# Kernel tuning notes

Hardware: AMD Instinct MI355X
Metric: run time of the kernel (lower is better)

Reference implementation:

```python
import math
import jax, jax.numpy as jnp
import numpy as np

E = 1024
H = 16
HD = E // H
MLP = 4 * E
EPS = 1e-6


def setup_inputs() -> dict:
    key = jax.random.key(0)
    ks = jax.random.split(key, 12)
    s = lambda fan_in: 1.0 / math.sqrt(fan_in)
    return {
        "x": jax.random.normal(ks[0], (8, 1024, E), dtype=jnp.float32),
        "ln1_g": jnp.ones((E,), jnp.float32),
        "ln1_b": jnp.zeros((E,), jnp.float32),
        "w_qkv": jax.random.normal(ks[1], (E, 3 * E), jnp.float32) * s(E),
        "b_qkv": jnp.zeros((3 * E,), jnp.float32),
        "w_o": jax.random.normal(ks[2], (E, E), jnp.float32) * s(E),
        "b_o": jnp.zeros((E,), jnp.float32),
        "ln2_g": jnp.ones((E,), jnp.float32),
        "ln2_b": jnp.zeros((E,), jnp.float32),
        "w_fc1": jax.random.normal(ks[3], (E, MLP), jnp.float32) * s(E),
        "b_fc1": jnp.zeros((MLP,), jnp.float32),
        "w_fc2": jax.random.normal(ks[4], (MLP, E), jnp.float32) * s(MLP),
        "b_fc2": jnp.zeros((E,), jnp.float32),
    }


def _layernorm(x, g, b):
    mu = jnp.mean(x, axis=-1, keepdims=True)
    var = jnp.mean(jnp.square(x - mu), axis=-1, keepdims=True)
    return (x - mu) * jax.lax.rsqrt(var + EPS) * g + b


def _attn(x, w_qkv, b_qkv, w_o, b_o):
    B, N, _ = x.shape
    qkv = (x @ w_qkv + b_qkv).reshape(B, N, 3, H, HD)
    q, k, v = qkv[:, :, 0], qkv[:, :, 1], qkv[:, :, 2]  # [B,N,H,HD]
    scores = jnp.einsum("bnhd,bmhd->bhnm", q, k) / math.sqrt(HD)
    probs = jax.nn.softmax(scores, axis=-1)
    out = jnp.einsum("bhnm,bmhd->bnhd", probs, v).reshape(B, N, H * HD)
    return out @ w_o + b_o


def reference(x, ln1_g, ln1_b, w_qkv, b_qkv, w_o, b_o, ln2_g, ln2_b,
              w_fc1, b_fc1, w_fc2, b_fc2):
    # pre-LN attention block with residual
    x = x + _attn(_layernorm(x, ln1_g, ln1_b), w_qkv, b_qkv, w_o, b_o)
    # pre-LN MLP block with residual (exact GELU, matching torch nn.GELU)
    h = _layernorm(x, ln2_g, ln2_b) @ w_fc1 + b_fc1
    h = jax.nn.gelu(h, approximate=False)
    x = x + (h @ w_fc2 + b_fc2)
    return x
```

## Files before the change

### kernel.cpp

```cpp
#include <hip/hip_runtime.h>
#include <stdint.h>

typedef unsigned short u16;
typedef __bf16 bf16x8 __attribute__((ext_vector_type(8)));
typedef float f32x4 __attribute__((ext_vector_type(4)));

#define GLD16(gp, lp) __builtin_amdgcn_global_load_lds( \
    (__attribute__((address_space(1))) void*)(uintptr_t)(gp), \
    (__attribute__((address_space(3))) void*)(uintptr_t)(lp), 16, 0, 0)

#define MM(a, b, c) __builtin_amdgcn_mfma_f32_16x16x32_bf16(a, b, c, 0, 0, 0)

__device__ __forceinline__ u16 f2bf(float f) {
  uint32_t u = __builtin_bit_cast(uint32_t, f);
  u += 0x7FFFu + ((u >> 16) & 1u);
  return (u16)(u >> 16);
}

__global__ __launch_bounds__(256) void wtrans(const float* __restrict__ w,
                                              u16* __restrict__ wt, int K, int Nn) {
  __shared__ float tile[64][68];
  const int c0 = blockIdx.x << 6, r0 = blockIdx.y << 6;
  const int t = threadIdx.x, tr = t >> 2, tc = t & 3;
#pragma unroll
  for (int p = 0; p < 4; ++p) {
    float4 v = *(const float4*)&w[(size_t)(r0 + tr) * Nn + c0 + tc * 4 + p * 16];
    tile[tr][tc * 4 + p * 16 + 0] = v.x;
    tile[tr][tc * 4 + p * 16 + 1] = v.y;
    tile[tr][tc * 4 + p * 16 + 2] = v.z;
    tile[tr][tc * 4 + p * 16 + 3] = v.w;
  }
  __syncthreads();
#pragma unroll
  for (int p = 0; p < 4; ++p) {
    u16 e0 = f2bf(tile[tc * 4 + p * 16 + 0][tr]);
    u16 e1 = f2bf(tile[tc * 4 + p * 16 + 1][tr]);
    u16 e2 = f2bf(tile[tc * 4 + p * 16 + 2][tr]);
    u16 e3 = f2bf(tile[tc * 4 + p * 16 + 3][tr]);
    uint2 o;
    o.x = (uint32_t)e0 | ((uint32_t)e1 << 16);
    o.y = (uint32_t)e2 | ((uint32_t)e3 << 16);
    *(uint2*)&wt[(size_t)(c0 + tr) * K + r0 + tc * 4 + p * 16] = o;
  }
}

__global__ __launch_bounds__(256) void lnorm(const float* x, const float* __restrict__ g,
                                             const float* __restrict__ bta,
                                             u16* __restrict__ out) {
  const int lane = threadIdx.x & 63, wid = threadIdx.x >> 6;
  const size_t token = (size_t)blockIdx.x * 4 + wid;
  const float* row = x + token * 1024;
  float v[16];
#pragma unroll
  for (int i = 0; i < 4; ++i) {
    float4 f = *(const float4*)&row[(lane + i * 64) * 4];
    v[i * 4 + 0] = f.x; v[i * 4 + 1] = f.y; v[i * 4 + 2] = f.z; v[i * 4 + 3] = f.w;
  }
  float s = 0.f, s2 = 0.f;
#pragma unroll
  for (int i = 0; i < 16; ++i) { s += v[i]; s2 += v[i] * v[i]; }
  for (int off = 1; off < 64; off <<= 1) {
    s += __shfl_xor(s, off);
    s2 += __shfl_xor(s2, off);
  }
  const float mu = s * (1.0f / 1024.0f);
  const float var = s2 * (1.0f / 1024.0f) - mu * mu;
  const float rstd = rsqrtf(var + 1e-6f);
  u16* orow = out + token * 1024;
#pragma unroll
  for (int i = 0; i < 4; ++i) {
    const int c = (lane + i * 64) * 4;
    float4 gv = *(const float4*)&g[c];
    float4 bv = *(const float4*)&bta[c];
    u16 e0 = f2bf((v[i * 4 + 0] - mu) * rstd * gv.x + bv.x);
    u16 e1 = f2bf((v[i * 4 + 1] - mu) * rstd * gv.y + bv.y);
    u16 e2 = f2bf((v[i * 4 + 2] - mu) * rstd * gv.z + bv.z);
    u16 e3 = f2bf((v[i * 4 + 3] - mu) * rstd * gv.w + bv.w);
    uint2 o;
    o.x = (uint32_t)e0 | ((uint32_t)e1 << 16);
    o.y = (uint32_t)e2 | ((uint32_t)e3 << 16);
    *(uint2*)&orow[c] = o;
  }
}

template <int EPI>
__global__ __launch_bounds__(256, 4) void g97(const u16* __restrict__ A,
                                              const u16* __restrict__ Bt,
                                              const float* __restrict__ bias,
                                              const float* res, void* Cout,
                                              int Ndim, int K, float qscale,
                                              int qlimit, int gn) {
  __shared__ __align__(16) u16 lds[2][8192];
  const int tid = threadIdx.x, lane = tid & 63, wid = tid >> 6;
  const int wm = wid & 1, wn = wid >> 1;

  const int wg = blockIdx.x;
  const int swz = (wg & 7) * ((int)gridDim.x >> 3) + (wg >> 3);
  const int mblk = swz / gn, nb = swz - mblk * gn;
  const int m0 = mblk << 7, n0 = nb << 7;

  const int srow = tid >> 2;
  const int gsub = (tid & 3) ^ ((tid >> 3) & 3);
  const u16* Ag = A + (size_t)(m0 + srow) * K + gsub * 8;
  const u16* Bg = Bt + (size_t)(n0 + srow) * K + gsub * 8;
  const size_t rstep = (size_t)64 * K;
  char* lb = (char*)&lds[0][0];

  const int rrow = lane & 15, g = lane >> 4;
  const int xg = g ^ ((rrow >> 1) & 3);
  const int aoff = (wm * 64 + rrow) * 64 + xg * 16;
  const int boff = 8192 + (wn * 64 + rrow) * 64 + xg * 16;

  const f32x4 fzero = {0.f, 0.f, 0.f, 0.f};
  f32x4 acc[4][4];
#pragma unroll
  for (int i = 0; i < 4; ++i)
#pragma unroll
    for (int j = 0; j < 4; ++j) acc[i][j] = fzero;

#define STG(kt, s) do { \
    char* d_ = lb + (s) * 16384; \
    GLD16(Ag + (size_t)(kt) * 32, d_ + tid * 16); \
    GLD16(Ag + rstep + (size_t)(kt) * 32, d_ + 4096 + tid * 16); \
    GLD16(Bg + (size_t)(kt) * 32, d_ + 8192 + tid * 16); \
    GLD16(Bg + rstep + (size_t)(kt) * 32, d_ + 12288 + tid * 16); \
  } while (0)

  const int nk = K >> 5;
  STG(0, 0);
  __syncthreads();
  for (int kt = 0; kt < nk; ++kt) {
    if (kt + 1 < nk) STG(kt + 1, (kt + 1) & 1);
    const char* sb = lb + (kt & 1) * 16384;
    bf16x8 af[4], bfr[4];
#pragma unroll
    for (int mf = 0; mf < 4; ++mf)
      af[mf] = *(const bf16x8*)(sb + aoff + mf * 1024);
#pragma unroll
    for (int nf = 0; nf < 4; ++nf)
      bfr[nf] = *(const bf16x8*)(sb + boff + nf * 1024);
#pragma unroll
    for (int mf = 0; mf < 4; ++mf)
#pragma unroll
      for (int nf = 0; nf < 4; ++nf)
        acc[mf][nf] = MM(af[mf], bfr[nf], acc[mf][nf]);
    __syncthreads();
  }
#undef STG

  const int g4 = (lane >> 4) << 2;
#pragma unroll
  for (int nf = 0; nf < 4; ++nf) {
    const int col = n0 + wn * 64 + nf * 16 + rrow;
    const float bvb = bias[col];
    const float csf = (EPI == 0 && col < qlimit) ? qscale : 1.0f;
#pragma unroll
    for (int mf = 0; mf < 4; ++mf) {
#pragma unroll
      for (int r = 0; r < 4; ++r) {
        const int row = m0 + wm * 64 + mf * 16 + g4 + r;
        float v = acc[mf][nf][r] + bvb;
        if (EPI == 0) v *= csf;
        if (EPI == 1) v = 0.5f * v * (1.0f + erff(v * 0.70710678118654752f));
        if (EPI == 2) {
          v += res[(size_t)row * Ndim + col];
          ((float*)Cout)[(size_t)row * Ndim + col] = v;
        } else {
          ((u16*)Cout)[(size_t)row * Ndim + col] = f2bf(v);
        }
      }
    }
  }
}

__global__ __launch_bounds__(256) void vtrans(const u16* __restrict__ qkv,
                                              u16* __restrict__ vt) {
  const int bh = blockIdx.y, b = bh >> 4, h = bh & 15;
  const int n0 = blockIdx.x << 6;
  __shared__ __align__(16) u16 tile[64][72];
  const int t = threadIdx.x, r = t >> 2, c = t & 3;
  const u16* src = qkv + (size_t)((b << 10) + n0 + r) * 3072 + 2048 + (h << 6);
#pragma unroll
  for (int p = 0; p < 2; ++p)
    *(uint4*)&tile[r][(c * 2 + p) * 8] = *(const uint4*)(src + (c * 2 + p) * 8);
  __syncthreads();
  u16* dst = vt + (size_t)((bh << 6) + r) * 1024 + n0;
#pragma unroll
  for (int p = 0; p < 2; ++p) {
    u16 o[8];
#pragma unroll
    for (int j = 0; j < 8; ++j) o[j] = tile[(c * 2 + p) * 8 + j][r];
    uint4 w;
    w.x = (uint32_t)o[0] | ((uint32_t)o[1] << 16);
    w.y = (uint32_t)o[2] | ((uint32_t)o[3] << 16);
    w.z = (uint32_t)o[4] | ((uint32_t)o[5] << 16);
    w.w = (uint32_t)o[6] | ((uint32_t)o[7] << 16);
    *(uint4*)&dst[(c * 2 + p) * 8] = w;
  }
}

__global__ __launch_bounds__(256) void attn64(const u16* __restrict__ qkv,
                                              const u16* __restrict__ vt,
                                              u16* __restrict__ aout) {
  const int bh = blockIdx.y, b = bh >> 4, h = bh & 15;
  const int q0 = blockIdx.x << 6;
  const int tid = threadIdx.x, lane = tid & 63, wid = tid >> 6;
  __shared__ __align__(16) u16 kl[4096];
  __shared__ __align__(16) u16 vl[4096];
  __shared__ __align__(16) u16 pl[4][1152];

  const int rrow = lane & 15;
  const int g = lane >> 4;
  const u16* qrow = qkv + (size_t)((b << 10) + q0 + (wid << 4) + rrow) * 3072 + (h << 6);
  bf16x8 qf0 = *(const bf16x8*)(qrow + (g << 3));
  bf16x8 qf1 = *(const bf16x8*)(qrow + 32 + (g << 3));

  const int sr = lane >> 3;
  const int lc = (lane & 7) ^ sr;
  const u16* kbase = qkv + (size_t)(b << 10) * 3072 + 1024 + (h << 6) +
                     (size_t)(16 * wid + sr) * 3072 + lc * 8;
  const u16* vbase = vt + (size_t)(bh << 6) * 1024 + (size_t)(16 * wid + sr) * 1024 + lc * 8;

  const f32x4 fzero = {0.f, 0.f, 0.f, 0.f};
  f32x4 oacc[4];
#pragma unroll
  for (int i = 0; i < 4; ++i) oacc[i] = fzero;
  f32x4 lacc = fzero;
  const int rcb = lane & 7;
  u16* plw = &pl[wid][0];

  for (int t = 0; t < 16; ++t) {
    const int kt0 = t << 6;
    GLD16(kbase + (size_t)kt0 * 3072, &kl[(2 * wid + 0) * 512]);
    GLD16(kbase + (size_t)kt0 * 3072 + 8 * 3072, &kl[(2 * wid + 1) * 512]);
    GLD16(vbase + kt0, &vl[(2 * wid + 0) * 512]);
    GLD16(vbase + kt0 + 8 * 1024, &vl[(2 * wid + 1) * 512]);
    __syncthreads();

    f32x4 s4[4];
#pragma unroll
    for (int i = 0; i < 4; ++i) s4[i] = fzero;
#pragma unroll
    for (int nf = 0; nf < 4; ++nf) {
      bf16x8 k0 = *(const bf16x8*)((const char*)kl + (nf * 16 + rrow) * 128 +
                                   ((g + 0) ^ rcb) * 16);
      bf16x8 k1 = *(const bf16x8*)((const char*)kl + (nf * 16 + rrow) * 128 +
                                   ((g + 4) ^ rcb) * 16);
      s4[nf] = __builtin_amdgcn_mfma_f32_16x16x32_bf16(k0, qf0, s4[nf], 0, 0, 0);
      s4[nf] = __builtin_amdgcn_mfma_f32_16x16x32_bf16(k1, qf1, s4[nf], 0, 0, 0);
    }

#pragma unroll
    for (int nf = 0; nf < 4; ++nf) {
      float p0 = exp2f(s4[nf][0]);
      float p1 = exp2f(s4[nf][1]);
      float p2 = exp2f(s4[nf][2]);
      float p3 = exp2f(s4[nf][3]);
      f32x4 pv = {p0, p1, p2, p3};
      lacc += pv;
      uint32_t a0 = __builtin_bit_cast(uint32_t, p0) + 0x8000u;
      uint32_t a1 = __builtin_bit_cast(uint32_t, p1) + 0x8000u;
      uint32_t a2 = __builtin_bit_cast(uint32_t, p2) + 0x8000u;
      uint32_t a3 = __builtin_bit_cast(uint32_t, p3) + 0x8000u;
      uint2 w;
      w.x = __builtin_amdgcn_perm(a1, a0, 0x07060302);
      w.y = __builtin_amdgcn_perm(a3, a2, 0x07060302);
      *(uint2*)(plw + rrow * 72 + nf * 16 + (g << 2)) = w;
    }

    bf16x8 pf0 = *(const bf16x8*)((const char*)plw + rrow * 144 + (g << 4));
    bf16x8 pf1 = *(const bf16x8*)((const char*)plw + rrow * 144 + (g << 4) + 64);
#pragma unroll
    for (int nf = 0; nf < 4; ++nf) {
      bf16x8 v0 = *(const bf16x8*)((const char*)vl + (nf * 16 + rrow) * 128 +
                                   ((g + 0) ^ rcb) * 16);
      bf16x8 v1 = *(const bf16x8*)((const char*)vl + (nf * 16 + rrow) * 128 +
                                   ((g + 4) ^ rcb) * 16);
      oacc[nf] = __builtin_amdgcn_mfma_f32_16x16x32_bf16(pf0, v0, oacc[nf], 0, 0, 0);
      oacc[nf] = __builtin_amdgcn_mfma_f32_16x16x32_bf16(pf1, v1, oacc[nf], 0, 0, 0);
    }
    __syncthreads();
  }

  float lsum = lacc[0] + lacc[1] + lacc[2] + lacc[3];
  lsum += __shfl_xor(lsum, 16);
  lsum += __shfl_xor(lsum, 32);
  const float inv = 1.0f / lsum;
  float invq[4];
#pragma unroll
  for (int r = 0; r < 4; ++r) {
    int bi = __builtin_amdgcn_ds_bpermute(((g << 2) + r) << 2,
                                          __builtin_bit_cast(int, inv));
    invq[r] = __builtin_bit_cast(float, bi);
  }
  u16* ob = aout + (size_t)((b << 10) + q0 + (wid << 4)) * 1024 + (h << 6);
#pragma unroll
  for (int nf = 0; nf < 4; ++nf)
#pragma unroll
    for (int r = 0; r < 4; ++r)
      ob[(size_t)(g * 4 + r) * 1024 + nf * 16 + rrow] = f2bf(oacc[nf][r] * invq[r]);
}

extern "C" void kernel_launch(void* const* d_in, const int* in_sizes, int n_in,
                              void* d_out, int out_size, void* d_ws, size_t ws_size,
                              hipStream_t stream) {
  const float* x = (const float*)d_in[0];
  const float* ln1_g = (const float*)d_in[1];
  const float* ln1_b = (const float*)d_in[2];
  const float* w_qkv = (const float*)d_in[3];
  const float* b_qkv = (const float*)d_in[4];
  const float* w_o = (const float*)d_in[5];
  const float* b_o = (const float*)d_in[6];
  const float* ln2_g = (const float*)d_in[7];
  const float* ln2_b = (const float*)d_in[8];
  const float* w_fc1 = (const float*)d_in[9];
  const float* b_fc1 = (const float*)d_in[10];
  const float* w_fc2 = (const float*)d_in[11];
  const float* b_fc2 = (const float*)d_in[12];
  float* out = (float*)d_out;

  char* w = (char*)d_ws;
  u16* wqkvT = (u16*)w; w += (size_t)3072 * 1024 * 2;
  u16* woT   = (u16*)w; w += (size_t)1024 * 1024 * 2;
  u16* wfc1T = (u16*)w; w += (size_t)4096 * 1024 * 2;
  u16* wfc2T = (u16*)w; w += (size_t)1024 * 4096 * 2;
  u16* xn    = (u16*)w; w += (size_t)8192 * 1024 * 2;
  u16* qkvb  = (u16*)w; w += (size_t)8192 * 3072 * 2;
  u16* vtb   = (u16*)w; w += (size_t)128 * 64 * 1024 * 2;
  u16* attnb = (u16*)w; w += (size_t)8192 * 1024 * 2;
  u16* hbuf  = qkvb;

  const float QS = 0.18033688011112042f;

  wtrans<<<dim3(48, 16), 256, 0, stream>>>(w_qkv, wqkvT, 1024, 3072);
  wtrans<<<dim3(16, 16), 256, 0, stream>>>(w_o, woT, 1024, 1024);
  wtrans<<<dim3(64, 16), 256, 0, stream>>>(w_fc1, wfc1T, 1024, 4096);
  wtrans<<<dim3(16, 64), 256, 0, stream>>>(w_fc2, wfc2T, 4096, 1024);

  lnorm<<<2048, 256, 0, stream>>>(x, ln1_g, ln1_b, xn);
  g97<0><<<1536, 256, 0, stream>>>(xn, wqkvT, b_qkv, nullptr, qkvb, 3072, 1024, QS, 1024, 24);
  vtrans<<<dim3(16, 128), 256, 0, stream>>>(qkvb, vtb);
  attn64<<<dim3(16, 128), 256, 0, stream>>>(qkvb, vtb, attnb);
  g97<2><<<512, 256, 0, stream>>>(attnb, woT, b_o, x, out, 1024, 1024, 1.f, 0, 8);
  lnorm<<<2048, 256, 0, stream>>>(out, ln2_g, ln2_b, xn);
  g97<1><<<2048, 256, 0, stream>>>(xn, wfc1T, b_fc1, nullptr, hbuf, 4096, 1024, 1.f, 0, 32);
  g97<2><<<512, 256, 0, stream>>>(hbuf, wfc2T, b_fc2, out, out, 1024, 4096, 1.f, 0, 8);
}
```

Measured before the change: 414.1 us.

## Double GEMM K-tile depth to 64 with wider swizzled LDS layout

The bf16 GEMM kernel now stages a K-slice of 64 per iteration instead of 32. Each iteration's tile doubles to 32 KB of LDS per buffer, with a new 8-chunk XOR swizzle and two MFMA sub-steps. This halves the number of loop iterations and __syncthreads barriers per output tile, amortizing sync and issue overhead. In exchange, LDS use grows to 64 KB per block and the launch-bounds occupancy hint drops from 4 to 2 blocks per CU, which reduces latency hiding.

```diff
diff --git a/kernel.cpp b/kernel.cpp
--- a/kernel.cpp
+++ b/kernel.cpp
@@ -84,13 +84,13 @@
 }
 
 template <int EPI>
-__global__ __launch_bounds__(256, 4) void g97(const u16* __restrict__ A,
+__global__ __launch_bounds__(256, 2) void g97(const u16* __restrict__ A,
                                               const u16* __restrict__ Bt,
                                               const float* __restrict__ bias,
                                               const float* res, void* Cout,
                                               int Ndim, int K, float qscale,
                                               int qlimit, int gn) {
-  __shared__ __align__(16) u16 lds[2][8192];
+  __shared__ __align__(16) u16 lds[2][16384];
   const int tid = threadIdx.x, lane = tid & 63, wid = tid >> 6;
   const int wm = wid & 1, wn = wid >> 1;
 
@@ -99,17 +99,19 @@
   const int mblk = swz / gn, nb = swz - mblk * gn;
   const int m0 = mblk << 7, n0 = nb << 7;
 
-  const int srow = tid >> 2;
-  const int gsub = (tid & 3) ^ ((tid >> 3) & 3);
-  const u16* Ag = A + (size_t)(m0 + srow) * K + gsub * 8;
-  const u16* Bg = Bt + (size_t)(n0 + srow) * K + gsub * 8;
-  const size_t rstep = (size_t)64 * K;
+  const int srow = tid >> 3;
+  const int schunk = (tid & 7) ^ (srow & 7);
+  const u16* Ag = A + (size_t)(m0 + srow) * K + schunk * 8;
+  const u16* Bg = Bt + (size_t)(n0 + srow) * K + schunk * 8;
+  const size_t rstep = (size_t)32 * K;
   char* lb = (char*)&lds[0][0];
 
   const int rrow = lane & 15, g = lane >> 4;
-  const int xg = g ^ ((rrow >> 1) & 3);
-  const int aoff = (wm * 64 + rrow) * 64 + xg * 16;
-  const int boff = 8192 + (wn * 64 + rrow) * 64 + xg * 16;
+  const int ph0 = (g ^ (rrow & 7)) * 16;
+  const int aoff0 = (wm * 64 + rrow) * 128 + ph0;
+  const int aoff1 = (wm * 64 + rrow) * 128 + (ph0 ^ 64);
+  const int boff0 = 16384 + (wn * 64 + rrow) * 128 + ph0;
+  const int boff1 = 16384 + (wn * 64 + rrow) * 128 + (ph0 ^ 64);
 
   const f32x4 fzero = {0.f, 0.f, 0.f, 0.f};
   f32x4 acc[4][4];
@@ -119,26 +121,43 @@
     for (int j = 0; j < 4; ++j) acc[i][j] = fzero;
 
 #define STG(kt, s) do { \
-    char* d_ = lb + (s) * 16384; \
-    GLD16(Ag + (size_t)(kt) * 32, d_ + tid * 16); \
-    GLD16(Ag + rstep + (size_t)(kt) * 32, d_ + 4096 + tid * 16); \
-    GLD16(Bg + (size_t)(kt) * 32, d_ + 8192 + tid * 16); \
-    GLD16(Bg + rstep + (size_t)(kt) * 32, d_ + 12288 + tid * 16); \
+    char* d_ = lb + (s) * 32768; \
+    const u16* a_ = Ag + (size_t)(kt) * 64; \
+    const u16* b_ = Bg + (size_t)(kt) * 64; \
+    GLD16(a_,             d_ + tid * 16); \
+    GLD16(a_ + rstep,     d_ + 4096 + tid * 16); \
+    GLD16(a_ + 2 * rstep, d_ + 8192 + tid * 16); \
+    GLD16(a_ + 3 * rstep, d_ + 12288 + tid * 16); \
+    GLD16(b_,             d_ + 16384 + tid * 16); \
+    GLD16(b_ + rstep,     d_ + 20480 + tid * 16); \
+    GLD16(b_ + 2 * rstep, d_ + 24576 + tid * 16); \
+    GLD16(b_ + 3 * rstep, d_ + 28672 + tid * 16); \
   } while (0)
 
-  const int nk = K >> 5;
+  const int nk = K >> 6;
   STG(0, 0);
   __syncthreads();
   for (int kt = 0; kt < nk; ++kt) {
     if (kt + 1 < nk) STG(kt + 1, (kt + 1) & 1);
-    const char* sb = lb + (kt & 1) * 16384;
+    const char* sb = lb + (kt & 1) * 32768;
     bf16x8 af[4], bfr[4];
 #pragma unroll
     for (int mf = 0; mf < 4; ++mf)
-      af[mf] = *(const bf16x8*)(sb + aoff + mf * 1024);
+      af[mf] = *(const bf16x8*)(sb + aoff0 + mf * 2048);
 #pragma unroll
     for (int nf = 0; nf < 4; ++nf)
-      bfr[nf] = *(const bf16x8*)(sb + boff + nf * 1024);
+      bfr[nf] = *(const bf16x8*)(sb + boff0 + nf * 2048);
+#pragma unroll
+    for (int mf = 0; mf < 4; ++mf)
+#pragma unroll
+      for (int nf = 0; nf < 4; ++nf)
+        acc[mf][nf] = MM(af[mf], bfr[nf], acc[mf][nf]);
+#pragma unroll
+    for (int mf = 0; mf < 4; ++mf)
+      af[mf] = *(const bf16x8*)(sb + aoff1 + mf * 2048);
+#pragma unroll
+    for (int nf = 0; nf < 4; ++nf)
+      bfr[nf] = *(const bf16x8*)(sb + boff1 + nf * 2048);
 #pragma unroll
     for (int mf = 0; mf < 4; ++mf)
 #pragma unroll
```

New measurement: 408.6 us. About the same (-1.3%).

## Restructure GEMM to 2-wave blocks with A fragments from global and double-buffer attention K/V

Applied to the files above, without the earlier changes.

The GEMM kernel now uses 128 threads (2 waves). Each wave computes a 128x64 tile, loading A fragments straight from global memory into registers and staging only B in LDS, with a 64-wide K step and register double-buffering of A. The attention kernel double-buffers its K/V LDS tiles so the next tile's loads overlap compute, removing one barrier per iteration. The intent is to cut LDS traffic and barrier stalls. The cost is doubled accumulator registers, uncoalesced per-lane global A reads, and fewer waves per block, which may hurt latency hiding.

```diff
diff --git a/kernel.cpp b/kernel.cpp
--- a/kernel.cpp
+++ b/kernel.cpp
@@ -84,81 +84,100 @@
 }
 
 template <int EPI>
-__global__ __launch_bounds__(256, 4) void g97(const u16* __restrict__ A,
-                                              const u16* __restrict__ Bt,
-                                              const float* __restrict__ bias,
-                                              const float* res, void* Cout,
-                                              int Ndim, int K, float qscale,
-                                              int qlimit, int gn) {
-  __shared__ __align__(16) u16 lds[2][8192];
-  const int tid = threadIdx.x, lane = tid & 63, wid = tid >> 6;
-  const int wm = wid & 1, wn = wid >> 1;
+__global__ __launch_bounds__(128, 2) void gflat(const u16* __restrict__ A,
+                                                const u16* __restrict__ Bt,
+                                                const float* __restrict__ bias,
+                                                const float* res, void* Cout,
+                                                int Ndim, int K, float qscale,
+                                                int qlimit, int gn) {
+  __shared__ __align__(16) u16 ldsB[2][8192];
+  const int tid = threadIdx.x, lane = tid & 63, wn = tid >> 6;
 
   const int wg = blockIdx.x;
   const int swz = (wg & 7) * ((int)gridDim.x >> 3) + (wg >> 3);
   const int mblk = swz / gn, nb = swz - mblk * gn;
   const int m0 = mblk << 7, n0 = nb << 7;
 
-  const int srow = tid >> 2;
-  const int gsub = (tid & 3) ^ ((tid >> 3) & 3);
-  const u16* Ag = A + (size_t)(m0 + srow) * K + gsub * 8;
-  const u16* Bg = Bt + (size_t)(n0 + srow) * K + gsub * 8;
-  const size_t rstep = (size_t)64 * K;
-  char* lb = (char*)&lds[0][0];
+  const int srow = tid >> 3;
+  const int schunk = (tid & 7) ^ ((tid >> 3) & 7);
+  const u16* Bg = Bt + (size_t)(n0 + srow) * K + schunk * 8;
+  const size_t brstep = (size_t)16 * K;
 
   const int rrow = lane & 15, g = lane >> 4;
-  const int xg = g ^ ((rrow >> 1) & 3);
-  const int aoff = (wm * 64 + rrow) * 64 + xg * 16;
-  const int boff = 8192 + (wn * 64 + rrow) * 64 + xg * 16;
+  const int boff0 = (wn * 64 + rrow) * 128 + ((g ^ (rrow & 7)) * 16);
+  const int boff1 = boff0 ^ 64;
+  const u16* Ab = A + (size_t)(m0 + rrow) * K + g * 8;
+  const size_t afstep = (size_t)16 * K;
 
   const f32x4 fzero = {0.f, 0.f, 0.f, 0.f};
-  f32x4 acc[4][4];
-#pragma unroll
-  for (int i = 0; i < 4; ++i)
+  f32x4 acc[8][4];
+#pragma unroll
+  for (int i = 0; i < 8; ++i)
 #pragma unroll
     for (int j = 0; j < 4; ++j) acc[i][j] = fzero;
 
-#define STG(kt, s) do { \
-    char* d_ = lb + (s) * 16384; \
-    GLD16(Ag + (size_t)(kt) * 32, d_ + tid * 16); \
-    GLD16(Ag + rstep + (size_t)(kt) * 32, d_ + 4096 + tid * 16); \
-    GLD16(Bg + (size_t)(kt) * 32, d_ + 8192 + tid * 16); \
-    GLD16(Bg + rstep + (size_t)(kt) * 32, d_ + 12288 + tid * 16); \
+#define STGB(kt, s) do { \
+    char* d_ = (char*)&ldsB[s][0]; \
+    const u16* b_ = Bg + (size_t)(kt) * 64; \
+    GLD16(b_ + 0 * brstep, d_ + 0 * 2048 + tid * 16); \
+    GLD16(b_ + 1 * brstep, d_ + 1 * 2048 + tid * 16); \
+    GLD16(b_ + 2 * brstep, d_ + 2 * 2048 + tid * 16); \
+    GLD16(b_ + 3 * brstep, d_ + 3 * 2048 + tid * 16); \
+    GLD16(b_ + 4 * brstep, d_ + 4 * 2048 + tid * 16); \
+    GLD16(b_ + 5 * brstep, d_ + 5 * 2048 + tid * 16); \
+    GLD16(b_ + 6 * brstep, d_ + 6 * 2048 + tid * 16); \
+    GLD16(b_ + 7 * brstep, d_ + 7 * 2048 + tid * 16); \
   } while (0)
 
-  const int nk = K >> 5;
-  STG(0, 0);
+#define LDA(arr, kc) do { \
+    const u16* ap_ = Ab + (size_t)(kc) * 32; \
+    _Pragma("unroll") \
+    for (int mf_ = 0; mf_ < 8; ++mf_) arr[mf_] = *(const uint4*)(ap_ + mf_ * afstep); \
+  } while (0)
+
+#define MMPH(arr, bbase) do { \
+    bf16x8 bf_[4]; \
+    _Pragma("unroll") \
+    for (int nf_ = 0; nf_ < 4; ++nf_) \
+      bf_[nf_] = *(const bf16x8*)(sb + (bbase) + nf_ * 2048); \
+    _Pragma("unroll") \
+    for (int mf_ = 0; mf_ < 8; ++mf_) { \
+      bf16x8 av_ = __builtin_bit_cast(bf16x8, arr[mf_]); \
+      _Pragma("unroll") \
+      for (int nf_ = 0; nf_ < 4; ++nf_) \
+        acc[mf_][nf_] = MM(av_, bf_[nf_], acc[mf_][nf_]); \
+    } \
+  } while (0)
+
+  uint4 a0[8], a1[8];
+  const int nk = K >> 6;
+  STGB(0, 0);
+  LDA(a0, 0);
   __syncthreads();
   for (int kt = 0; kt < nk; ++kt) {
-    if (kt + 1 < nk) STG(kt + 1, (kt + 1) & 1);
-    const char* sb = lb + (kt & 1) * 16384;
-    bf16x8 af[4], bfr[4];
-#pragma unroll
-    for (int mf = 0; mf < 4; ++mf)
-      af[mf] = *(const bf16x8*)(sb + aoff + mf * 1024);
-#pragma unroll
-    for (int nf = 0; nf < 4; ++nf)
-      bfr[nf] = *(const bf16x8*)(sb + boff + nf * 1024);
-#pragma unroll
-    for (int mf = 0; mf < 4; ++mf)
-#pragma unroll
-      for (int nf = 0; nf < 4; ++nf)
-        acc[mf][nf] = MM(af[mf], bfr[nf], acc[mf][nf]);
+    if (kt + 1 < nk) STGB(kt + 1, (kt + 1) & 1);
+    LDA(a1, 2 * kt + 1);
+    const char* sb = (const char*)&ldsB[kt & 1][0];
+    MMPH(a0, boff0);
+    if (kt + 1 < nk) LDA(a0, 2 * kt + 2);
+    MMPH(a1, boff1);
     __syncthreads();
   }
-#undef STG
-
-  const int g4 = (lane >> 4) << 2;
+#undef STGB
+#undef LDA
+#undef MMPH
+
+  const int g4 = g << 2;
 #pragma unroll
   for (int nf = 0; nf < 4; ++nf) {
     const int col = n0 + wn * 64 + nf * 16 + rrow;
     const float bvb = bias[col];
     const float csf = (EPI == 0 && col < qlimit) ? qscale : 1.0f;
 #pragma unroll
-    for (int mf = 0; mf < 4; ++mf) {
+    for (int mf = 0; mf < 8; ++mf) {
 #pragma unroll
       for (int r = 0; r < 4; ++r) {
-        const int row = m0 + wm * 64 + mf * 16 + g4 + r;
+        const int row = m0 + mf * 16 + g4 + r;
         float v = acc[mf][nf][r] + bvb;
         if (EPI == 0) v *= csf;
         if (EPI == 1) v = 0.5f * v * (1.0f + erff(v * 0.70710678118654752f));
@@ -205,8 +224,8 @@
   const int bh = blockIdx.y, b = bh >> 4, h = bh & 15;
   const int q0 = blockIdx.x << 6;
   const int tid = threadIdx.x, lane = tid & 63, wid = tid >> 6;
-  __shared__ __align__(16) u16 kl[4096];
-  __shared__ __align__(16) u16 vl[4096];
+  __shared__ __align__(16) u16 kl[2][4096];
+  __shared__ __align__(16) u16 vl[2][4096];
   __shared__ __align__(16) u16 pl[4][1152];
 
   const int rrow = lane & 15;
@@ -229,23 +248,28 @@
   const int rcb = lane & 7;
   u16* plw = &pl[wid][0];
 
+#define ASTAGE(t, s) do { \
+    const int kt0_ = (t) << 6; \
+    GLD16(kbase + (size_t)kt0_ * 3072, &kl[s][(2 * wid + 0) * 512]); \
+    GLD16(kbase + (size_t)kt0_ * 3072 + 8 * 3072, &kl[s][(2 * wid + 1) * 512]); \
+    GLD16(vbase + kt0_, &vl[s][(2 * wid + 0) * 512]); \
+    GLD16(vbase + kt0_ + 8 * 1024, &vl[s][(2 * wid + 1) * 512]); \
+  } while (0)
+
+  ASTAGE(0, 0);
+  __syncthreads();
   for (int t = 0; t < 16; ++t) {
-    const int kt0 = t << 6;
-    GLD16(kbase + (size_t)kt0 * 3072, &kl[(2 * wid + 0) * 512]);
-    GLD16(kbase + (size_t)kt0 * 3072 + 8 * 3072, &kl[(2 * wid + 1) * 512]);
-    GLD16(vbase + kt0, &vl[(2 * wid + 0) * 512]);
-    GLD16(vbase + kt0 + 8 * 1024, &vl[(2 * wid + 1) * 512]);
-    __syncthreads();
+    if (t + 1 < 16) ASTAGE(t + 1, (t + 1) & 1);
+    const char* klp = (const char*)&kl[t & 1][0];
+    const char* vlp = (const char*)&vl[t & 1][0];
 
     f32x4 s4[4];
 #pragma unroll
     for (int i = 0; i < 4; ++i) s4[i] = fzero;
 #pragma unroll
     for (int nf = 0; nf < 4; ++nf) {
-      bf16x8 k0 = *(const bf16x8*)((const char*)kl + (nf * 16 + rrow) * 128 +
-                                   ((g + 0) ^ rcb) * 16);
-      bf16x8 k1 = *(const bf16x8*)((const char*)kl + (nf * 16 + rrow) * 128 +
-                                   ((g + 4) ^ rcb) * 16);
+      bf16x8 k0 = *(const bf16x8*)(klp + (nf * 16 + rrow) * 128 + ((g + 0) ^ rcb) * 16);
+      bf16x8 k1 = *(const bf16x8*)(klp + (nf * 16 + rrow) * 128 + ((g + 4) ^ rcb) * 16);
       s4[nf] = __builtin_amdgcn_mfma_f32_16x16x32_bf16(k0, qf0, s4[nf], 0, 0, 0);
       s4[nf] = __builtin_amdgcn_mfma_f32_16x16x32_bf16(k1, qf1, s4[nf], 0, 0, 0);
     }
@@ -272,15 +296,14 @@
     bf16x8 pf1 = *(const bf16x8*)((const char*)plw + rrow * 144 + (g << 4) + 64);
 #pragma unroll
     for (int nf = 0; nf < 4; ++nf) {
-      bf16x8 v0 = *(const bf16x8*)((const char*)vl + (nf * 16 + rrow) * 128 +
-                                   ((g + 0) ^ rcb) * 16);
-      bf16x8 v1 = *(const bf16x8*)((const char*)vl + (nf * 16 + rrow) * 128 +
-                                   ((g + 4) ^ rcb) * 16);
+      bf16x8 v0 = *(const bf16x8*)(vlp + (nf * 16 + rrow) * 128 + ((g + 0) ^ rcb) * 16);
+      bf16x8 v1 = *(const bf16x8*)(vlp + (nf * 16 + rrow) * 128 + ((g + 4) ^ rcb) * 16);
       oacc[nf] = __builtin_amdgcn_mfma_f32_16x16x32_bf16(pf0, v0, oacc[nf], 0, 0, 0);
       oacc[nf] = __builtin_amdgcn_mfma_f32_16x16x32_bf16(pf1, v1, oacc[nf], 0, 0, 0);
     }
     __syncthreads();
   }
+#undef ASTAGE
 
   float lsum = lacc[0] + lacc[1] + lacc[2] + lacc[3];
   lsum += __shfl_xor(lsum, 16);
@@ -338,11 +361,11 @@
   wtrans<<<dim3(16, 64), 256, 0, stream>>>(w_fc2, wfc2T, 4096, 1024);
 
   lnorm<<<2048, 256, 0, stream>>>(x, ln1_g, ln1_b, xn);
-  g97<0><<<1536, 256, 0, stream>>>(xn, wqkvT, b_qkv, nullptr, qkvb, 3072, 1024, QS, 1024, 24);
+  gflat<0><<<1536, 128, 0, stream>>>(xn, wqkvT, b_qkv, nullptr, qkvb, 3072, 1024, QS, 1024, 24);
   vtrans<<<dim3(16, 128), 256, 0, stream>>>(qkvb, vtb);
   attn64<<<dim3(16, 128), 256, 0, stream>>>(qkvb, vtb, attnb);
-  g97<2><<<512, 256, 0, stream>>>(attnb, woT, b_o, x, out, 1024, 1024, 1.f, 0, 8);
+  gflat<2><<<512, 128, 0, stream>>>(attnb, woT, b_o, x, out, 1024, 1024, 1.f, 0, 8);
   lnorm<<<2048, 256, 0, stream>>>(out, ln2_g, ln2_b, xn);
-  g97<1><<<2048, 256, 0, stream>>>(xn, wfc1T, b_fc1, nullptr, hbuf, 4096, 1024, 1.f, 0, 32);
-  g97<2><<<512, 256, 0, stream>>>(hbuf, wfc2T, b_fc2, out, out, 1024, 4096, 1.f, 0, 8);
-}
+  gflat<1><<<2048, 128, 0, stream>>>(xn, wfc1T, b_fc1, nullptr, hbuf, 4096, 1024, 1.f, 0, 32);
+  gflat<2><<<512, 128, 0, stream>>>(hbuf, wfc2T, b_fc2, out, out, 1024, 4096, 1.f, 0, 8);
+}
```

Result: slower. 684.3 us (+65.2%).

## Enlarge GEMM tile to 256x128 and double-buffer attention K/V loads

Applied to the files above, without the earlier changes.

The GEMM kernel now computes a 256x128 output tile per block, with each wave covering 128x64 (8x4 MFMA fragments). This raises arithmetic intensity per LDS load and halves the grid sizes, at the cost of more accumulator registers and lower occupancy (launch bounds drop to 2 blocks per CU). Separately, the attention kernel double-buffers its K/V LDS tiles so the next tile's global-to-LDS loads overlap the current tile's compute. With only 256 blocks, the Wo and fc2 GEMMs may leave some of the 256 CUs underfilled.

```diff
diff --git a/kernel.cpp b/kernel.cpp
--- a/kernel.cpp
+++ b/kernel.cpp
@@ -84,20 +84,20 @@
 }
 
 template <int EPI>
-__global__ __launch_bounds__(256, 4) void g97(const u16* __restrict__ A,
+__global__ __launch_bounds__(256, 2) void gwt(const u16* __restrict__ A,
                                               const u16* __restrict__ Bt,
                                               const float* __restrict__ bias,
                                               const float* res, void* Cout,
                                               int Ndim, int K, float qscale,
                                               int qlimit, int gn) {
-  __shared__ __align__(16) u16 lds[2][8192];
+  __shared__ __align__(16) u16 lds[2][12288];
   const int tid = threadIdx.x, lane = tid & 63, wid = tid >> 6;
-  const int wm = wid & 1, wn = wid >> 1;
+  const int wm = wid >> 1, wn = wid & 1;
 
   const int wg = blockIdx.x;
   const int swz = (wg & 7) * ((int)gridDim.x >> 3) + (wg >> 3);
   const int mblk = swz / gn, nb = swz - mblk * gn;
-  const int m0 = mblk << 7, n0 = nb << 7;
+  const int m0 = mblk << 8, n0 = nb << 7;
 
   const int srow = tid >> 2;
   const int gsub = (tid & 3) ^ ((tid >> 3) & 3);
@@ -107,23 +107,27 @@
   char* lb = (char*)&lds[0][0];
 
   const int rrow = lane & 15, g = lane >> 4;
-  const int xg = g ^ ((rrow >> 1) & 3);
-  const int aoff = (wm * 64 + rrow) * 64 + xg * 16;
-  const int boff = 8192 + (wn * 64 + rrow) * 64 + xg * 16;
+  const int xg = (g ^ ((rrow >> 1) & 3)) * 16;
+  const int aoff = wm * 8192 + rrow * 64 + xg;
+  const int boff = 16384 + wn * 4096 + rrow * 64 + xg;
 
   const f32x4 fzero = {0.f, 0.f, 0.f, 0.f};
-  f32x4 acc[4][4];
-#pragma unroll
-  for (int i = 0; i < 4; ++i)
+  f32x4 acc[8][4];
+#pragma unroll
+  for (int i = 0; i < 8; ++i)
 #pragma unroll
     for (int j = 0; j < 4; ++j) acc[i][j] = fzero;
 
 #define STG(kt, s) do { \
-    char* d_ = lb + (s) * 16384; \
-    GLD16(Ag + (size_t)(kt) * 32, d_ + tid * 16); \
-    GLD16(Ag + rstep + (size_t)(kt) * 32, d_ + 4096 + tid * 16); \
-    GLD16(Bg + (size_t)(kt) * 32, d_ + 8192 + tid * 16); \
-    GLD16(Bg + rstep + (size_t)(kt) * 32, d_ + 12288 + tid * 16); \
+    char* d_ = lb + (s) * 24576; \
+    const u16* a_ = Ag + (size_t)(kt) * 32; \
+    const u16* b_ = Bg + (size_t)(kt) * 32; \
+    GLD16(a_,             d_ + tid * 16); \
+    GLD16(a_ + rstep,     d_ + 4096 + tid * 16); \
+    GLD16(a_ + 2 * rstep, d_ + 8192 + tid * 16); \
+    GLD16(a_ + 3 * rstep, d_ + 12288 + tid * 16); \
+    GLD16(b_,             d_ + 16384 + tid * 16); \
+    GLD16(b_ + rstep,     d_ + 20480 + tid * 16); \
   } while (0)
 
   const int nk = K >> 5;
@@ -131,16 +135,16 @@
   __syncthreads();
   for (int kt = 0; kt < nk; ++kt) {
     if (kt + 1 < nk) STG(kt + 1, (kt + 1) & 1);
-    const char* sb = lb + (kt & 1) * 16384;
-    bf16x8 af[4], bfr[4];
-#pragma unroll
-    for (int mf = 0; mf < 4; ++mf)
-      af[mf] = *(const bf16x8*)(sb + aoff + mf * 1024);
+    const char* sb = lb + (kt & 1) * 24576;
+    bf16x8 bfr[4], af[8];
 #pragma unroll
     for (int nf = 0; nf < 4; ++nf)
       bfr[nf] = *(const bf16x8*)(sb + boff + nf * 1024);
 #pragma unroll
-    for (int mf = 0; mf < 4; ++mf)
+    for (int mf = 0; mf < 8; ++mf)
+      af[mf] = *(const bf16x8*)(sb + aoff + mf * 1024);
+#pragma unroll
+    for (int mf = 0; mf < 8; ++mf)
 #pragma unroll
       for (int nf = 0; nf < 4; ++nf)
         acc[mf][nf] = MM(af[mf], bfr[nf], acc[mf][nf]);
@@ -148,17 +152,17 @@
   }
 #undef STG
 
-  const int g4 = (lane >> 4) << 2;
+  const int g4 = g << 2;
 #pragma unroll
   for (int nf = 0; nf < 4; ++nf) {
     const int col = n0 + wn * 64 + nf * 16 + rrow;
     const float bvb = bias[col];
     const float csf = (EPI == 0 && col < qlimit) ? qscale : 1.0f;
 #pragma unroll
-    for (int mf = 0; mf < 4; ++mf) {
+    for (int mf = 0; mf < 8; ++mf) {
 #pragma unroll
       for (int r = 0; r < 4; ++r) {
-        const int row = m0 + wm * 64 + mf * 16 + g4 + r;
+        const int row = m0 + wm * 128 + mf * 16 + g4 + r;
         float v = acc[mf][nf][r] + bvb;
         if (EPI == 0) v *= csf;
         if (EPI == 1) v = 0.5f * v * (1.0f + erff(v * 0.70710678118654752f));
@@ -205,8 +209,8 @@
   const int bh = blockIdx.y, b = bh >> 4, h = bh & 15;
   const int q0 = blockIdx.x << 6;
   const int tid = threadIdx.x, lane = tid & 63, wid = tid >> 6;
-  __shared__ __align__(16) u16 kl[4096];
-  __shared__ __align__(16) u16 vl[4096];
+  __shared__ __align__(16) u16 kl[2][4096];
+  __shared__ __align__(16) u16 vl[2][4096];
   __shared__ __align__(16) u16 pl[4][1152];
 
   const int rrow = lane & 15;
@@ -229,23 +233,28 @@
   const int rcb = lane & 7;
   u16* plw = &pl[wid][0];
 
+#define ASTAGE(t, s) do { \
+    const int kt0_ = (t) << 6; \
+    GLD16(kbase + (size_t)kt0_ * 3072, &kl[s][(2 * wid + 0) * 512]); \
+    GLD16(kbase + (size_t)kt0_ * 3072 + 8 * 3072, &kl[s][(2 * wid + 1) * 512]); \
+    GLD16(vbase + kt0_, &vl[s][(2 * wid + 0) * 512]); \
+    GLD16(vbase + kt0_ + 8 * 1024, &vl[s][(2 * wid + 1) * 512]); \
+  } while (0)
+
+  ASTAGE(0, 0);
+  __syncthreads();
   for (int t = 0; t < 16; ++t) {
-    const int kt0 = t << 6;
-    GLD16(kbase + (size_t)kt0 * 3072, &kl[(2 * wid + 0) * 512]);
-    GLD16(kbase + (size_t)kt0 * 3072 + 8 * 3072, &kl[(2 * wid + 1) * 512]);
-    GLD16(vbase + kt0, &vl[(2 * wid + 0) * 512]);
-    GLD16(vbase + kt0 + 8 * 1024, &vl[(2 * wid + 1) * 512]);
-    __syncthreads();
+    if (t + 1 < 16) ASTAGE(t + 1, (t + 1) & 1);
+    const char* klp = (const char*)&kl[t & 1][0];
+    const char* vlp = (const char*)&vl[t & 1][0];
 
     f32x4 s4[4];
 #pragma unroll
     for (int i = 0; i < 4; ++i) s4[i] = fzero;
 #pragma unroll
     for (int nf = 0; nf < 4; ++nf) {
-      bf16x8 k0 = *(const bf16x8*)((const char*)kl + (nf * 16 + rrow) * 128 +
-                                   ((g + 0) ^ rcb) * 16);
-      bf16x8 k1 = *(const bf16x8*)((const char*)kl + (nf * 16 + rrow) * 128 +
-                                   ((g + 4) ^ rcb) * 16);
+      bf16x8 k0 = *(const bf16x8*)(klp + (nf * 16 + rrow) * 128 + ((g + 0) ^ rcb) * 16);
+      bf16x8 k1 = *(const bf16x8*)(klp + (nf * 16 + rrow) * 128 + ((g + 4) ^ rcb) * 16);
       s4[nf] = __builtin_amdgcn_mfma_f32_16x16x32_bf16(k0, qf0, s4[nf], 0, 0, 0);
       s4[nf] = __builtin_amdgcn_mfma_f32_16x16x32_bf16(k1, qf1, s4[nf], 0, 0, 0);
     }
@@ -272,15 +281,14 @@
     bf16x8 pf1 = *(const bf16x8*)((const char*)plw + rrow * 144 + (g << 4) + 64);
 #pragma unroll
     for (int nf = 0; nf < 4; ++nf) {
-      bf16x8 v0 = *(const bf16x8*)((const char*)vl + (nf * 16 + rrow) * 128 +
-                                   ((g + 0) ^ rcb) * 16);
-      bf16x8 v1 = *(const bf16x8*)((const char*)vl + (nf * 16 + rrow) * 128 +
-                                   ((g + 4) ^ rcb) * 16);
+      bf16x8 v0 = *(const bf16x8*)(vlp + (nf * 16 + rrow) * 128 + ((g + 0) ^ rcb) * 16);
+      bf16x8 v1 = *(const bf16x8*)(vlp + (nf * 16 + rrow) * 128 + ((g + 4) ^ rcb) * 16);
       oacc[nf] = __builtin_amdgcn_mfma_f32_16x16x32_bf16(pf0, v0, oacc[nf], 0, 0, 0);
       oacc[nf] = __builtin_amdgcn_mfma_f32_16x16x32_bf16(pf1, v1, oacc[nf], 0, 0, 0);
     }
     __syncthreads();
   }
+#undef ASTAGE
 
   float lsum = lacc[0] + lacc[1] + lacc[2] + lacc[3];
   lsum += __shfl_xor(lsum, 16);
@@ -338,11 +346,11 @@
   wtrans<<<dim3(16, 64), 256, 0, stream>>>(w_fc2, wfc2T, 4096, 1024);
 
   lnorm<<<2048, 256, 0, stream>>>(x, ln1_g, ln1_b, xn);
-  g97<0><<<1536, 256, 0, stream>>>(xn, wqkvT, b_qkv, nullptr, qkvb, 3072, 1024, QS, 1024, 24);
+  gwt<0><<<768, 256, 0, stream>>>(xn, wqkvT, b_qkv, nullptr, qkvb, 3072, 1024, QS, 1024, 24);
   vtrans<<<dim3(16, 128), 256, 0, stream>>>(qkvb, vtb);
   attn64<<<dim3(16, 128), 256, 0, stream>>>(qkvb, vtb, attnb);
-  g97<2><<<512, 256, 0, stream>>>(attnb, woT, b_o, x, out, 1024, 1024, 1.f, 0, 8);
+  gwt<2><<<256, 256, 0, stream>>>(attnb, woT, b_o, x, out, 1024, 1024, 1.f, 0, 8);
   lnorm<<<2048, 256, 0, stream>>>(out, ln2_g, ln2_b, xn);
-  g97<1><<<2048, 256, 0, stream>>>(xn, wfc1T, b_fc1, nullptr, hbuf, 4096, 1024, 1.f, 0, 32);
-  g97<2><<<512, 256, 0, stream>>>(hbuf, wfc2T, b_fc2, out, out, 1024, 4096, 1.f, 0, 8);
-}
+  gwt<1><<<1024, 256, 0, stream>>>(xn, wfc1T, b_fc1, nullptr, hbuf, 4096, 1024, 1.f, 0, 32);
+  gwt<2><<<256, 256, 0, stream>>>(hbuf, wfc2T, b_fc2, out, out, 1024, 4096, 1.f, 0, 8);
+}
```

After: 452.5 us. 1.09x slower.
